# Performance work log

Measured on AMD Instinct MI355X. Metric: run time of the kernel, lower is better.

Reference implementation:

```python
import math
import jax, jax.numpy as jnp
import numpy as np

B, S, D = 4, 4096, 1024
H = 16
DH = D // H          # 64
INNER = H * DH       # 1024
EPS = 1e-6


def _layernorm(z, g, b):
    m = jnp.mean(z, axis=-1, keepdims=True)
    v = jnp.mean((z - m) ** 2, axis=-1, keepdims=True)
    return (z - m) * jax.lax.rsqrt(v + EPS) * g + b


def _pos_encoding(seq_len, d_model, dtype):
    pos = jnp.arange(seq_len, dtype=jnp.float32)[:, None]                    # [S,1]
    div = jnp.exp(jnp.arange(0, d_model, 2, dtype=jnp.float32)
                  * (-math.log(10000.0) / d_model))                          # [D/2]
    pe = jnp.zeros((seq_len, d_model), dtype=jnp.float32)
    pe = pe.at[:, 0::2].set(jnp.sin(pos * div))
    pe = pe.at[:, 1::2].set(jnp.cos(pos * div))
    return pe.astype(dtype)[None]                                            # [1,S,D]


def setup_inputs() -> dict:
    key = jax.random.key(0)
    ks = jax.random.split(key, 8)
    std = 0.02
    x = jax.random.normal(ks[0], (B, S, D), dtype=jnp.float32)
    inp = {
        "x": x,
        "ln1_g": jnp.ones((D,), jnp.float32),
        "ln1_b": jnp.zeros((D,), jnp.float32),
        "Wqkv": std * jax.random.normal(ks[1], (D, 3 * INNER), jnp.float32),
        "Wo": std * jax.random.normal(ks[2], (INNER, D), jnp.float32),
        "bo": jnp.zeros((D,), jnp.float32),
        "ln2_g": jnp.ones((D,), jnp.float32),
        "ln2_b": jnp.zeros((D,), jnp.float32),
        "W1": std * jax.random.normal(ks[3], (D, D), jnp.float32),
        "b1": jnp.zeros((D,), jnp.float32),
        "W2": std * jax.random.normal(ks[4], (D, D), jnp.float32),
        "b2": jnp.zeros((D,), jnp.float32),
    }
    return inp


def reference(x, ln1_g, ln1_b, Wqkv, Wo, bo, ln2_g, ln2_b, W1, b1, W2, b2):
    # --- ln_1 + positional encoding (dropout p=0) ---
    h = _layernorm(x, ln1_g, ln1_b)
    h = h + _pos_encoding(h.shape[1], h.shape[2], h.dtype)
    # --- linear self-attention (non-causal, efficient attention) ---
    qkv = h @ Wqkv                                                           # [B,S,3*INNER]
    q, k, v = jnp.split(qkv, 3, axis=-1)
    def heads(t):  # [B,S,INNER] -> [B,H,S,DH]
        return t.reshape(B, S, H, DH).transpose(0, 2, 1, 3)
    q, k, v = heads(q), heads(k), heads(v)
    q = jax.nn.softmax(q, axis=-1) * (DH ** -0.5)
    k = jax.nn.softmax(k, axis=-2)
    ctx = jnp.einsum("bhnd,bhne->bhde", k, v)                               # [B,H,DH,DH]
    attn_out = jnp.einsum("bhnd,bhde->bhne", q, ctx)                        # [B,H,S,DH]
    attn_out = attn_out.transpose(0, 2, 1, 3).reshape(B, S, INNER)
    attn_out = attn_out @ Wo + bo
    # --- residual, ln_2, MLP (Linear -> GELU -> Linear), residual ---
    x = x + attn_out
    y = _layernorm(x, ln2_g, ln2_b)
    y = jax.nn.gelu(y @ W1 + b1, approximate=False) @ W2 + b2
    return x + y
```

## Files before the change

### kernel.cpp

```cpp
#include <hip/hip_runtime.h>
#include <hip/hip_bf16.h>
#include <math.h>

#define B_   4
#define S_   4096
#define D_   1024
#define H_   16
#define DH_  64
#define BS_  (B_ * S_)
#define N3_  3072

using bf16 = __hip_bfloat16;
typedef __attribute__((ext_vector_type(8))) short bf16x8;
typedef __attribute__((ext_vector_type(4))) float f32x4;

#define GAS __attribute__((address_space(1)))
#define LAS __attribute__((address_space(3)))

__device__ __forceinline__ void gload_lds16(const bf16* g, bf16* l) {
  __builtin_amdgcn_global_load_lds((const GAS void*)g, (LAS void*)l, 16, 0, 0);
}

__device__ __forceinline__ float bf2f(short u) {
  unsigned int x = ((unsigned int)(unsigned short)u) << 16;
  return __builtin_bit_cast(float, x);
}
__device__ __forceinline__ unsigned short f2bfu(float f) {
  bf16 t = __float2bfloat16(f);
  return *(unsigned short*)&t;
}

__global__ __launch_bounds__(256)
void transpose_cast4(const float* __restrict__ Wqkv, const float* __restrict__ Wo,
                     const float* __restrict__ W1, const float* __restrict__ W2,
                     bf16* __restrict__ wqkvt, bf16* __restrict__ wot,
                     bf16* __restrict__ w1t, bf16* __restrict__ w2t)
{
  __shared__ float tile[32][33];
  int gx = blockIdx.x;
  const float* W; bf16* Wt; int N, xo;
  if (gx < 96)        { W = Wqkv; Wt = wqkvt; N = N3_; xo = gx; }
  else if (gx < 128)  { W = Wo;   Wt = wot;   N = D_;  xo = gx - 96; }
  else if (gx < 160)  { W = W1;   Wt = w1t;   N = D_;  xo = gx - 128; }
  else                { W = W2;   Wt = w2t;   N = D_;  xo = gx - 160; }
  int n0 = xo * 32, k0 = blockIdx.y * 32;
  int tx = threadIdx.x & 31, ty = threadIdx.x >> 5;
#pragma unroll
  for (int j = 0; j < 32; j += 8)
    tile[ty + j][tx] = W[(size_t)(k0 + ty + j) * N + n0 + tx];
  __syncthreads();
#pragma unroll
  for (int j = 0; j < 32; j += 8)
    Wt[(size_t)(n0 + ty + j) * 1024 + k0 + tx] = __float2bfloat16(tile[tx][ty + j]);
}

template<bool PE, bool INBF16>
__global__ __launch_bounds__(256)
void ln_kernel(const float* __restrict__ Xf, const bf16* __restrict__ Xb,
               const float* __restrict__ G, const float* __restrict__ Bv,
               bf16* __restrict__ out)
{
  int row = blockIdx.x;
  int t = threadIdx.x;
  float4 v;
  if (INBF16) {
    ushort4 u = ((const ushort4*)Xb)[(size_t)row * (D_ / 4) + t];
    v.x = bf2f(u.x); v.y = bf2f(u.y); v.z = bf2f(u.z); v.w = bf2f(u.w);
  } else {
    v = ((const float4*)(Xf + (size_t)row * D_))[t];
  }
  float s  = v.x + v.y + v.z + v.w;
  float ss = v.x * v.x + v.y * v.y + v.z * v.z + v.w * v.w;
#pragma unroll
  for (int o = 32; o > 0; o >>= 1) { s += __shfl_xor(s, o); ss += __shfl_xor(ss, o); }
  __shared__ float red[8];
  int wid = t >> 6, lane = t & 63;
  if (lane == 0) { red[wid] = s; red[4 + wid] = ss; }
  __syncthreads();
  s  = red[0] + red[1] + red[2] + red[3];
  ss = red[4] + red[5] + red[6] + red[7];
  float mean = s * (1.0f / D_);
  float var  = ss * (1.0f / D_) - mean * mean;
  float rs   = rsqrtf(var + 1e-6f);
  int d0 = t * 4;
  const float4 g4 = ((const float4*)G)[t];
  const float4 b4 = ((const float4*)Bv)[t];
  float o0 = (v.x - mean) * rs * g4.x + b4.x;
  float o1 = (v.y - mean) * rs * g4.y + b4.y;
  float o2 = (v.z - mean) * rs * g4.z + b4.z;
  float o3 = (v.w - mean) * rs * g4.w + b4.w;
  if (PE) {
    const float C = -0.0089944730194f;
    float p = (float)(row & (S_ - 1));
    float sn, cs;
    __sincosf(p * __expf((float)d0 * C), &sn, &cs);        o0 += sn; o1 += cs;
    __sincosf(p * __expf((float)(d0 + 2) * C), &sn, &cs);  o2 += sn; o3 += cs;
  }
  ushort4 pk;
  pk.x = f2bfu(o0); pk.y = f2bfu(o1); pk.z = f2bfu(o2); pk.w = f2bfu(o3);
  ((ushort4*)out)[(size_t)row * (D_ / 4) + t] = pk;
}

enum { EPI_QKV = 0, EPI_BIAS_RES_BF16 = 1, EPI_BIAS_GELU_BF16 = 2, EPI_BIAS_RESB_F32 = 3 };

#define MFMA_ __builtin_amdgcn_mfma_f32_16x16x32_bf16

template<int EPI, bool AHM>
__global__ __launch_bounds__(512)
void gemm256(const bf16* __restrict__ A, const bf16* __restrict__ Bt,
             float* __restrict__ Cf, bf16* __restrict__ Cb,
             const float* __restrict__ bias, const float* __restrict__ resf,
             const bf16* __restrict__ resb,
             bf16* __restrict__ Ck, bf16* __restrict__ Cv,
             int M, int N, int K)
{
  extern __shared__ __align__(16) char smem[];
  bf16* lds = (bf16*)smem;

  const int t = threadIdx.x;
  const int wid = t >> 6, lane = t & 63;
  const int wr = wid >> 2, wc = wid & 3;
  const int bid = blockIdx.x;
  const int c = bid & 7;
  const int w = bid >> 3;
  const int sst = w >> 4;
  const int ii = w & 15;
  const int txg = sst >> 1, tyg = sst & 1;
  const int iy = ii & 3, ix = ii >> 2;
  const int ty = c * 8 + tyg * 4 + iy;
  const int tx = txg * 4 + ix;
  const int m0 = ty << 8, n0 = tx << 8;

  const bf16* Ab = AHM
      ? A + (((size_t)(m0 >> 12) * 16) * 4096 + (m0 & 4095)) * 64
      : A + (size_t)m0 * K;
  const bf16* Bb = Bt + (size_t)n0 * K;

  const int srow = t >> 2;
  const int scol = (((t & 3) ^ ((t >> 3) & 3)) * 8);
  const int NT = K >> 6;
  const int fr = lane & 15;
  const int fksw = (((lane >> 4) ^ ((lane >> 1) & 3)) * 8);

  f32x4 acc[8][4] = {};

  #define LDSHALF(b, mat, kh) (lds + (((((b) << 1) + (mat)) << 1) + (kh)) * 8192)

  #define STAGE(kt, mat, kh) do {                                              \
    bf16* _dst = LDSHALF((kt) & 1, (mat), (kh)) + t * 8;                       \
    const int _ktk = (kt) & (NT - 1);                                          \
    if ((mat) == 0 && AHM) {                                                   \
      const bf16* _sb = Ab + (size_t)_ktk * 262144 + (size_t)srow * 64         \
                        + (kh) * 32 + scol;                                    \
      gload_lds16(_sb, _dst);                                                  \
      gload_lds16(_sb + 8192, _dst + 4096);                                    \
    } else {                                                                   \
      const bf16* _sb = ((mat) == 0 ? Ab : Bb) + (size_t)srow * K              \
                        + (_ktk << 6) + (kh) * 32 + scol;                      \
      gload_lds16(_sb, _dst);                                                  \
      gload_lds16(_sb + (size_t)128 * K, _dst + 4096);                         \
    }                                                                          \
  } while (0)

  STAGE(0, 0, 0); STAGE(0, 1, 0);
  STAGE(0, 0, 1); STAGE(0, 1, 1);
  asm volatile("s_waitcnt vmcnt(4)" ::: "memory");
  __builtin_amdgcn_s_barrier();

#pragma unroll 2
  for (int kt = 0; kt < NT; ++kt) {
    const int cur = kt & 1;
    const bf16* hA0 = LDSHALF(cur, 0, 0);
    const bf16* hB0 = LDSHALF(cur, 1, 0);
    const bf16* hA1 = LDSHALF(cur, 0, 1);
    const bf16* hB1 = LDSHALF(cur, 1, 1);
    bf16x8 a[8], b0, b1, b2, b3;

#pragma unroll
    for (int mi = 0; mi < 8; ++mi)
      a[mi] = *(const bf16x8*)&hA0[(wr * 128 + mi * 16 + fr) * 32 + fksw];
    b0 = *(const bf16x8*)&hB0[(wc * 64 +  0 + fr) * 32 + fksw];
    b1 = *(const bf16x8*)&hB0[(wc * 64 + 16 + fr) * 32 + fksw];
    STAGE(kt + 1, 0, 0);
    __builtin_amdgcn_s_barrier();
    __builtin_amdgcn_s_setprio(1);
#pragma unroll
    for (int mi = 0; mi < 8; ++mi) {
      acc[mi][0] = MFMA_(a[mi], b0, acc[mi][0], 0, 0, 0);
      acc[mi][1] = MFMA_(a[mi], b1, acc[mi][1], 0, 0, 0);
    }
    __builtin_amdgcn_s_setprio(0);
    __builtin_amdgcn_s_barrier();

    b2 = *(const bf16x8*)&hB0[(wc * 64 + 32 + fr) * 32 + fksw];
    b3 = *(const bf16x8*)&hB0[(wc * 64 + 48 + fr) * 32 + fksw];
    STAGE(kt + 1, 1, 0);
    __builtin_amdgcn_s_barrier();
    __builtin_amdgcn_s_setprio(1);
#pragma unroll
    for (int mi = 0; mi < 8; ++mi) {
      acc[mi][2] = MFMA_(a[mi], b2, acc[mi][2], 0, 0, 0);
      acc[mi][3] = MFMA_(a[mi], b3, acc[mi][3], 0, 0, 0);
    }
    __builtin_amdgcn_s_setprio(0);
    asm volatile("s_waitcnt vmcnt(4)" ::: "memory");
    __builtin_amdgcn_s_barrier();

#pragma unroll
    for (int mi = 0; mi < 8; ++mi)
      a[mi] = *(const bf16x8*)&hA1[(wr * 128 + mi * 16 + fr) * 32 + fksw];
    b0 = *(const bf16x8*)&hB1[(wc * 64 +  0 + fr) * 32 + fksw];
    b1 = *(const bf16x8*)&hB1[(wc * 64 + 16 + fr) * 32 + fksw];
    STAGE(kt + 1, 0, 1);
    __builtin_amdgcn_s_barrier();
    __builtin_amdgcn_s_setprio(1);
#pragma unroll
    for (int mi = 0; mi < 8; ++mi) {
      acc[mi][0] = MFMA_(a[mi], b0, acc[mi][0], 0, 0, 0);
      acc[mi][1] = MFMA_(a[mi], b1, acc[mi][1], 0, 0, 0);
    }
    __builtin_amdgcn_s_setprio(0);
    __builtin_amdgcn_s_barrier();

    b2 = *(const bf16x8*)&hB1[(wc * 64 + 32 + fr) * 32 + fksw];
    b3 = *(const bf16x8*)&hB1[(wc * 64 + 48 + fr) * 32 + fksw];
    STAGE(kt + 1, 1, 1);
    __builtin_amdgcn_s_barrier();
    __builtin_amdgcn_s_setprio(1);
#pragma unroll
    for (int mi = 0; mi < 8; ++mi) {
      acc[mi][2] = MFMA_(a[mi], b2, acc[mi][2], 0, 0, 0);
      acc[mi][3] = MFMA_(a[mi], b3, acc[mi][3], 0, 0, 0);
    }
    __builtin_amdgcn_s_setprio(0);
    asm volatile("s_waitcnt vmcnt(4)" ::: "memory");
    __builtin_amdgcn_s_barrier();
  }
  asm volatile("s_waitcnt vmcnt(0)" ::: "memory");

  const int brow = m0 >> 12;
  const int mrow = m0 & 4095;
#pragma unroll
  for (int mi = 0; mi < 8; ++mi) {
    int rowb = m0 + wr * 128 + mi * 16 + (lane >> 4) * 4;
#pragma unroll
    for (int ni = 0; ni < 4; ++ni) {
      int col = n0 + wc * 64 + ni * 16 + fr;
      if (EPI == EPI_QKV) {
        int qsel = col >> 10;
        int hh = (col >> 6) & 15;
        int dd = col & 63;
        int sloc = mrow + wr * 128 + mi * 16 + (lane >> 4) * 4;
        if (qsel == 0) {
          unsigned short* qp = (unsigned short*)Cb +
            (((size_t)(brow * 16 + hh) * 4096 + sloc) * 64 + dd);
#pragma unroll
          for (int j = 0; j < 4; ++j)
            qp[(size_t)j * 64] = f2bfu(acc[mi][ni][j]);
        } else {
          unsigned short* kp = (unsigned short*)(qsel == 1 ? Ck : Cv) +
            (((size_t)(brow * 16 + hh) * 64 + dd) * 4096 + sloc);
          ushort4 pk;
          pk.x = f2bfu(acc[mi][ni][0]); pk.y = f2bfu(acc[mi][ni][1]);
          pk.z = f2bfu(acc[mi][ni][2]); pk.w = f2bfu(acc[mi][ni][3]);
          *(ushort4*)kp = pk;
        }
      } else {
#pragma unroll
        for (int j = 0; j < 4; ++j) {
          int row = rowb + j;
          float v = acc[mi][ni][j];
          if (EPI == EPI_BIAS_RES_BF16) {
            Cb[(size_t)row * N + col] =
              __float2bfloat16(v + bias[col] + resf[(size_t)row * N + col]);
          } else if (EPI == EPI_BIAS_GELU_BF16) {
            float u = v + bias[col];
            u = 0.5f * u * (1.0f + erff(u * 0.70710678118654752f));
            Cb[(size_t)row * N + col] = __float2bfloat16(u);
          } else {
            Cf[(size_t)row * N + col] =
              v + bias[col] + bf2f(*(const short*)&resb[(size_t)row * N + col]);
          }
        }
      }
    }
  }
  #undef STAGE
  #undef LDSHALF
}

__global__ __launch_bounds__(256)
void ctx_partial(const bf16* __restrict__ kT, const bf16* __restrict__ vT,
                 float* __restrict__ pctx, float* __restrict__ pden)
{
  int blk = blockIdx.x;
  int kc = blk & 7, bh = blk >> 3;
  int t = threadIdx.x, lane = t & 63, wid = t >> 6;
  const int fr = lane & 15, g = lane >> 4;
  __shared__ float part[4][4096];
  __shared__ float dpart[4][64];

  f32x4 acc[4][4] = {};
  float dsum[4] = {0.f, 0.f, 0.f, 0.f};
  const unsigned short* kb = (const unsigned short*)kT + (size_t)bh * 64 * 4096;
  const unsigned short* vb = (const unsigned short*)vT + (size_t)bh * 64 * 4096;
  const int kbase = kc * 512 + wid * 128;
#pragma unroll
  for (int i = 0; i < 4; ++i) {
    int kofs = kbase + i * 32 + g * 8;
    bf16x8 av[4], bv[4];
#pragma unroll
    for (int mi = 0; mi < 4; ++mi) {
      bf16x8 kr = *(const bf16x8*)(kb + (size_t)(mi * 16 + fr) * 4096 + kofs);
      bf16x8 ae;
      float es = 0.f;
#pragma unroll
      for (int j = 0; j < 8; ++j) {
        float e = __expf(bf2f(kr[j]));
        es += e;
        ae[j] = (short)f2bfu(e);
      }
      dsum[mi] += es;
      av[mi] = ae;
      bv[mi] = *(const bf16x8*)(vb + (size_t)(mi * 16 + fr) * 4096 + kofs);
    }
#pragma unroll
    for (int mi = 0; mi < 4; ++mi)
#pragma unroll
      for (int ni = 0; ni < 4; ++ni)
        acc[mi][ni] = MFMA_(av[mi], bv[ni], acc[mi][ni], 0, 0, 0);
  }
#pragma unroll
  for (int mi = 0; mi < 4; ++mi) {
    dsum[mi] += __shfl_xor(dsum[mi], 16);
    dsum[mi] += __shfl_xor(dsum[mi], 32);
  }
#pragma unroll
  for (int mi = 0; mi < 4; ++mi)
#pragma unroll
    for (int ni = 0; ni < 4; ++ni)
      *(f32x4*)&part[wid][(mi * 4 + ni) * 256 + lane * 4] = acc[mi][ni];
  if (g == 0) {
#pragma unroll
    for (int mi = 0; mi < 4; ++mi) dpart[wid][mi * 16 + fr] = dsum[mi];
  }
  __syncthreads();
  int lane2 = t & 63, fg = t >> 6;
#pragma unroll
  for (int ff = 0; ff < 4; ++ff) {
    int f = fg * 4 + ff;
    f32x4 s = {};
#pragma unroll
    for (int ww = 0; ww < 4; ++ww)
      s += *(const f32x4*)&part[ww][f * 256 + lane2 * 4];
    *(f32x4*)&pctx[((size_t)blk * 16 + f) * 256 + lane2 * 4] = s;
  }
  if (t < 64)
    pden[blk * 64 + t] = dpart[0][t] + dpart[1][t] + dpart[2][t] + dpart[3][t];
}

__global__ __launch_bounds__(256)
void ctx_merge(const float* __restrict__ pctx, const float* __restrict__ pden,
               bf16* __restrict__ ctxT)
{
  int bh = blockIdx.x;
  int t = threadIdx.x, lane2 = t & 63, fg = t >> 6;
  __shared__ float rden[64];
  if (t < 64) {
    float s = 0.f;
    for (int kc = 0; kc < 8; ++kc) s += pden[(bh * 8 + kc) * 64 + t];
    rden[t] = 1.0f / s;
  }
  __syncthreads();
  int fr2 = lane2 & 15, g2 = lane2 >> 4;
#pragma unroll
  for (int ff = 0; ff < 4; ++ff) {
    int f = fg * 4 + ff;
    int mi = f >> 2, ni = f & 3;
    f32x4 s = {};
#pragma unroll
    for (int kc = 0; kc < 8; ++kc)
      s += *(const f32x4*)&pctx[(((size_t)(bh * 8 + kc)) * 16 + f) * 256 + lane2 * 4];
    int e = ni * 16 + fr2;
    int d0 = mi * 16 + g2 * 4;
    ushort4 pk;
    pk.x = f2bfu(s[0] * rden[d0 + 0]);
    pk.y = f2bfu(s[1] * rden[d0 + 1]);
    pk.z = f2bfu(s[2] * rden[d0 + 2]);
    pk.w = f2bfu(s[3] * rden[d0 + 3]);
    *(ushort4*)((unsigned short*)ctxT + ((size_t)bh * 64 + e) * 64 + d0) = pk;
  }
}

__global__ __launch_bounds__(256)
void attn_kernel(const bf16* __restrict__ qhm, const bf16* __restrict__ ctxT,
                 bf16* __restrict__ attn)
{
  int blk = blockIdx.x;
  int chunk = blk & 15, bh = blk >> 4;
  int t = threadIdx.x, lane = t & 63, wid = t >> 6;
  __shared__ bf16 P[256 * 64];
  __shared__ bf16 CT[64 * 64];

  {
    const unsigned short* cg = (const unsigned short*)ctxT + (size_t)bh * 4096;
#pragma unroll
    for (int r = 0; r < 2; ++r) {
      int idx = r * 256 + t;
      int e = idx >> 3, b = idx & 7;
      bf16x8 v = *(const bf16x8*)(cg + idx * 8);
      *(bf16x8*)&CT[e * 64 + ((b ^ (e & 7)) * 8)] = v;
    }
  }
  {
    int s = chunk * 256 + t;
    const unsigned short* qp = (const unsigned short*)qhm + ((size_t)bh * 4096 + s) * 64;
    float p[64];
#pragma unroll
    for (int j = 0; j < 8; ++j) {
      bf16x8 q8 = *(const bf16x8*)(qp + j * 8);
#pragma unroll
      for (int i = 0; i < 8; ++i) p[j * 8 + i] = bf2f(q8[i]);
    }
    float mx = p[0];
#pragma unroll
    for (int d = 1; d < 64; ++d) mx = fmaxf(mx, p[d]);
    float sum = 0.f;
#pragma unroll
    for (int d = 0; d < 64; ++d) { p[d] = __expf(p[d] - mx); sum += p[d]; }
    float f = 0.125f / sum;
    bf16* pb = &P[(t >> 6) * 4096 + (t & 63) * 64];
#pragma unroll
    for (int b = 0; b < 8; ++b) {
      bf16x8 pk;
#pragma unroll
      for (int i = 0; i < 8; ++i) pk[i] = (short)f2bfu(p[b * 8 + i] * f);
      *(bf16x8*)&pb[((b ^ (t & 7)) * 8)] = pk;
    }
  }
  __syncthreads();

  const int fr = lane & 15, g = lane >> 4;
  f32x4 acc[4][4] = {};
  const bf16* Pw = &P[wid * 4096];
#pragma unroll
  for (int ks = 0; ks < 2; ++ks) {
    bf16x8 av[4], bv[4];
#pragma unroll
    for (int mi = 0; mi < 4; ++mi) {
      int r = mi * 16 + fr;
      av[mi] = *(const bf16x8*)&Pw[r * 64 + (((ks * 4 + g) ^ (r & 7)) * 8)];
    }
#pragma unroll
    for (int ni = 0; ni < 4; ++ni) {
      int e = ni * 16 + fr;
      bv[ni] = *(const bf16x8*)&CT[e * 64 + (((ks * 4 + g) ^ (e & 7)) * 8)];
    }
#pragma unroll
    for (int mi = 0; mi < 4; ++mi)
#pragma unroll
      for (int ni = 0; ni < 4; ++ni)
        acc[mi][ni] = MFMA_(av[mi], bv[ni], acc[mi][ni], 0, 0, 0);
  }
  unsigned short* ob = (unsigned short*)attn +
      ((size_t)bh * 4096 + chunk * 256 + wid * 64) * 64;
#pragma unroll
  for (int mi = 0; mi < 4; ++mi)
#pragma unroll
    for (int ni = 0; ni < 4; ++ni) {
      int e = ni * 16 + fr;
#pragma unroll
      for (int j = 0; j < 4; ++j) {
        int r = mi * 16 + g * 4 + j;
        ob[(size_t)r * 64 + e] = f2bfu(acc[mi][ni][j]);
      }
    }
}

#define OFF_WQKVT  ((size_t)0)
#define OFF_WOT    ((size_t)6291456)
#define OFF_W1T    ((size_t)8388608)
#define OFF_W2T    ((size_t)10485760)
#define OFF_CTXT   ((size_t)12582912)
#define OFF_PCTX   ((size_t)13631488)
#define OFF_PDEN   ((size_t)22020096)
#define OFF_ATTN   ((size_t)33554432)
#define OFF_H      OFF_ATTN
#define OFF_QHM    ((size_t)67108864)
#define OFF_KT     ((size_t)100663296)
#define OFF_VT     ((size_t)134217728)
#define OFF_Z      OFF_QHM
#define OFF_X2B    OFF_KT
#define OFF_Y      OFF_VT

extern "C" void kernel_launch(void* const* d_in, const int* in_sizes, int n_in,
                              void* d_out, int out_size, void* d_ws, size_t ws_size,
                              hipStream_t stream)
{
  const float* x     = (const float*)d_in[0];
  const float* ln1_g = (const float*)d_in[1];
  const float* ln1_b = (const float*)d_in[2];
  const float* Wqkv  = (const float*)d_in[3];
  const float* Wo    = (const float*)d_in[4];
  const float* bo    = (const float*)d_in[5];
  const float* ln2_g = (const float*)d_in[6];
  const float* ln2_b = (const float*)d_in[7];
  const float* W1    = (const float*)d_in[8];
  const float* b1    = (const float*)d_in[9];
  const float* W2    = (const float*)d_in[10];
  const float* b2    = (const float*)d_in[11];
  float* out = (float*)d_out;
  char* ws = (char*)d_ws;

  bf16*  h     = (bf16*)(ws + OFF_H);
  bf16*  attn  = (bf16*)(ws + OFF_ATTN);
  bf16*  qhm   = (bf16*)(ws + OFF_QHM);
  bf16*  kT    = (bf16*)(ws + OFF_KT);
  bf16*  vT    = (bf16*)(ws + OFF_VT);
  bf16*  ctxT  = (bf16*)(ws + OFF_CTXT);
  float* pctx  = (float*)(ws + OFF_PCTX);
  float* pden  = (float*)(ws + OFF_PDEN);
  bf16*  x2b   = (bf16*)(ws + OFF_X2B);
  bf16*  y     = (bf16*)(ws + OFF_Y);
  bf16*  z     = (bf16*)(ws + OFF_Z);
  bf16*  wqkvt = (bf16*)(ws + OFF_WQKVT);
  bf16*  wot   = (bf16*)(ws + OFF_WOT);
  bf16*  w1t   = (bf16*)(ws + OFF_W1T);
  bf16*  w2t   = (bf16*)(ws + OFF_W2T);

  const size_t GEMM_LDS = 131072;

  transpose_cast4<<<dim3(192, 32), 256, 0, stream>>>(Wqkv, Wo, W1, W2,
                                                     wqkvt, wot, w1t, w2t);

  ln_kernel<true, false><<<BS_, 256, 0, stream>>>(x, nullptr, ln1_g, ln1_b, h);

  gemm256<EPI_QKV, false><<<(N3_ / 256) * (BS_ / 256), 512, GEMM_LDS, stream>>>(
      h, wqkvt, nullptr, qhm, nullptr, nullptr, nullptr, kT, vT, BS_, N3_, D_);

  ctx_partial<<<512, 256, 0, stream>>>(kT, vT, pctx, pden);
  ctx_merge<<<64, 256, 0, stream>>>(pctx, pden, ctxT);

  attn_kernel<<<1024, 256, 0, stream>>>(qhm, ctxT, attn);

  gemm256<EPI_BIAS_RES_BF16, true><<<(D_ / 256) * (BS_ / 256), 512, GEMM_LDS, stream>>>(
      attn, wot, nullptr, x2b, bo, x, nullptr, nullptr, nullptr, BS_, D_, D_);

  ln_kernel<false, true><<<BS_, 256, 0, stream>>>(nullptr, x2b, ln2_g, ln2_b, y);

  gemm256<EPI_BIAS_GELU_BF16, false><<<(D_ / 256) * (BS_ / 256), 512, GEMM_LDS, stream>>>(
      y, w1t, nullptr, z, b1, nullptr, nullptr, nullptr, nullptr, BS_, D_, D_);

  gemm256<EPI_BIAS_RESB_F32, false><<<(D_ / 256) * (BS_ / 256), 512, GEMM_LDS, stream>>>(
      z, w2t, out, nullptr, b2, nullptr, x2b, nullptr, nullptr, BS_, D_, D_);
}
```

Before: 353.6 us.

## Stage GEMM epilogues through LDS for vectorized stores; fuse LN1 with weight transpose

GEMM epilogues now write the bf16 accumulators into swizzled LDS, then read back rows of 8 elements so that bias, residual and GELU are applied and stored with 16-byte vector accesses instead of scalar strided writes. The Q part of the QKV GEMM uses the same path for head-major output. The first layernorm and the weight transpose-cast are merged into one launch. The prefetch index is clamped instead of wrapped. The trade-off is that intermediate results are rounded to bf16 before bias and residual are added, and the epilogue gains an extra LDS pass and a barrier.

```diff
diff --git a/kernel.cpp b/kernel.cpp
--- a/kernel.cpp
+++ b/kernel.cpp
@@ -31,44 +31,76 @@
 }
 
 __global__ __launch_bounds__(256)
-void transpose_cast4(const float* __restrict__ Wqkv, const float* __restrict__ Wo,
-                     const float* __restrict__ W1, const float* __restrict__ W2,
-                     bf16* __restrict__ wqkvt, bf16* __restrict__ wot,
-                     bf16* __restrict__ w1t, bf16* __restrict__ w2t)
+void prep_kernel(const float* __restrict__ x, const float* __restrict__ ln1_g,
+                 const float* __restrict__ ln1_b, bf16* __restrict__ h,
+                 const float* __restrict__ Wqkv, const float* __restrict__ Wo,
+                 const float* __restrict__ W1, const float* __restrict__ W2,
+                 bf16* __restrict__ wqkvt, bf16* __restrict__ wot,
+                 bf16* __restrict__ w1t, bf16* __restrict__ w2t)
 {
-  __shared__ float tile[32][33];
-  int gx = blockIdx.x;
-  const float* W; bf16* Wt; int N, xo;
-  if (gx < 96)        { W = Wqkv; Wt = wqkvt; N = N3_; xo = gx; }
-  else if (gx < 128)  { W = Wo;   Wt = wot;   N = D_;  xo = gx - 96; }
-  else if (gx < 160)  { W = W1;   Wt = w1t;   N = D_;  xo = gx - 128; }
-  else                { W = W2;   Wt = w2t;   N = D_;  xo = gx - 160; }
-  int n0 = xo * 32, k0 = blockIdx.y * 32;
-  int tx = threadIdx.x & 31, ty = threadIdx.x >> 5;
-#pragma unroll
-  for (int j = 0; j < 32; j += 8)
-    tile[ty + j][tx] = W[(size_t)(k0 + ty + j) * N + n0 + tx];
-  __syncthreads();
-#pragma unroll
-  for (int j = 0; j < 32; j += 8)
-    Wt[(size_t)(n0 + ty + j) * 1024 + k0 + tx] = __float2bfloat16(tile[tx][ty + j]);
-}
-
-template<bool PE, bool INBF16>
+  int bid = blockIdx.x;
+  int t = threadIdx.x;
+  if (bid < BS_) {
+    int row = bid;
+    float4 v = ((const float4*)(x + (size_t)row * D_))[t];
+    float s  = v.x + v.y + v.z + v.w;
+    float ss = v.x * v.x + v.y * v.y + v.z * v.z + v.w * v.w;
+#pragma unroll
+    for (int o = 32; o > 0; o >>= 1) { s += __shfl_xor(s, o); ss += __shfl_xor(ss, o); }
+    __shared__ float red[8];
+    int wid = t >> 6, lane = t & 63;
+    if (lane == 0) { red[wid] = s; red[4 + wid] = ss; }
+    __syncthreads();
+    s  = red[0] + red[1] + red[2] + red[3];
+    ss = red[4] + red[5] + red[6] + red[7];
+    float mean = s * (1.0f / D_);
+    float var  = ss * (1.0f / D_) - mean * mean;
+    float rs   = rsqrtf(var + 1e-6f);
+    int d0 = t * 4;
+    const float4 g4 = ((const float4*)ln1_g)[t];
+    const float4 b4 = ((const float4*)ln1_b)[t];
+    float o0 = (v.x - mean) * rs * g4.x + b4.x;
+    float o1 = (v.y - mean) * rs * g4.y + b4.y;
+    float o2 = (v.z - mean) * rs * g4.z + b4.z;
+    float o3 = (v.w - mean) * rs * g4.w + b4.w;
+    const float C = -0.0089944730194f;
+    float p = (float)(row & (S_ - 1));
+    float sn, cs;
+    __sincosf(p * __expf((float)d0 * C), &sn, &cs);        o0 += sn; o1 += cs;
+    __sincosf(p * __expf((float)(d0 + 2) * C), &sn, &cs);  o2 += sn; o3 += cs;
+    ushort4 pk;
+    pk.x = f2bfu(o0); pk.y = f2bfu(o1); pk.z = f2bfu(o2); pk.w = f2bfu(o3);
+    ((ushort4*)h)[(size_t)row * (D_ / 4) + t] = pk;
+  } else {
+    int e = bid - BS_;
+    int gx = e % 192, ky = e / 192;
+    __shared__ float tile[32][33];
+    const float* W; bf16* Wt; int N, xo;
+    if (gx < 96)        { W = Wqkv; Wt = wqkvt; N = N3_; xo = gx; }
+    else if (gx < 128)  { W = Wo;   Wt = wot;   N = D_;  xo = gx - 96; }
+    else if (gx < 160)  { W = W1;   Wt = w1t;   N = D_;  xo = gx - 128; }
+    else                { W = W2;   Wt = w2t;   N = D_;  xo = gx - 160; }
+    int n0 = xo * 32, k0 = ky * 32;
+    int tx = t & 31, ty = t >> 5;
+#pragma unroll
+    for (int j = 0; j < 32; j += 8)
+      tile[ty + j][tx] = W[(size_t)(k0 + ty + j) * N + n0 + tx];
+    __syncthreads();
+#pragma unroll
+    for (int j = 0; j < 32; j += 8)
+      Wt[(size_t)(n0 + ty + j) * 1024 + k0 + tx] = __float2bfloat16(tile[tx][ty + j]);
+  }
+}
+
 __global__ __launch_bounds__(256)
-void ln_kernel(const float* __restrict__ Xf, const bf16* __restrict__ Xb,
-               const float* __restrict__ G, const float* __restrict__ Bv,
-               bf16* __restrict__ out)
+void ln_kernel(const bf16* __restrict__ Xb, const float* __restrict__ G,
+               const float* __restrict__ Bv, bf16* __restrict__ out)
 {
   int row = blockIdx.x;
   int t = threadIdx.x;
+  ushort4 u = ((const ushort4*)Xb)[(size_t)row * (D_ / 4) + t];
   float4 v;
-  if (INBF16) {
-    ushort4 u = ((const ushort4*)Xb)[(size_t)row * (D_ / 4) + t];
-    v.x = bf2f(u.x); v.y = bf2f(u.y); v.z = bf2f(u.z); v.w = bf2f(u.w);
-  } else {
-    v = ((const float4*)(Xf + (size_t)row * D_))[t];
-  }
+  v.x = bf2f(u.x); v.y = bf2f(u.y); v.z = bf2f(u.z); v.w = bf2f(u.w);
   float s  = v.x + v.y + v.z + v.w;
   float ss = v.x * v.x + v.y * v.y + v.z * v.z + v.w * v.w;
 #pragma unroll
@@ -82,22 +114,13 @@
   float mean = s * (1.0f / D_);
   float var  = ss * (1.0f / D_) - mean * mean;
   float rs   = rsqrtf(var + 1e-6f);
-  int d0 = t * 4;
   const float4 g4 = ((const float4*)G)[t];
   const float4 b4 = ((const float4*)Bv)[t];
-  float o0 = (v.x - mean) * rs * g4.x + b4.x;
-  float o1 = (v.y - mean) * rs * g4.y + b4.y;
-  float o2 = (v.z - mean) * rs * g4.z + b4.z;
-  float o3 = (v.w - mean) * rs * g4.w + b4.w;
-  if (PE) {
-    const float C = -0.0089944730194f;
-    float p = (float)(row & (S_ - 1));
-    float sn, cs;
-    __sincosf(p * __expf((float)d0 * C), &sn, &cs);        o0 += sn; o1 += cs;
-    __sincosf(p * __expf((float)(d0 + 2) * C), &sn, &cs);  o2 += sn; o3 += cs;
-  }
   ushort4 pk;
-  pk.x = f2bfu(o0); pk.y = f2bfu(o1); pk.z = f2bfu(o2); pk.w = f2bfu(o3);
+  pk.x = f2bfu((v.x - mean) * rs * g4.x + b4.x);
+  pk.y = f2bfu((v.y - mean) * rs * g4.y + b4.y);
+  pk.z = f2bfu((v.z - mean) * rs * g4.z + b4.z);
+  pk.w = f2bfu((v.w - mean) * rs * g4.w + b4.w);
   ((ushort4*)out)[(size_t)row * (D_ / 4) + t] = pk;
 }
 
@@ -146,9 +169,9 @@
 
   #define LDSHALF(b, mat, kh) (lds + (((((b) << 1) + (mat)) << 1) + (kh)) * 8192)
 
-  #define STAGE(kt, mat, kh) do {                                              \
-    bf16* _dst = LDSHALF((kt) & 1, (mat), (kh)) + t * 8;                       \
-    const int _ktk = (kt) & (NT - 1);                                          \
+  #define STAGE(bkt, akt, mat, kh) do {                                        \
+    bf16* _dst = LDSHALF((bkt) & 1, (mat), (kh)) + t * 8;                      \
+    const int _ktk = (akt);                                                    \
     if ((mat) == 0 && AHM) {                                                   \
       const bf16* _sb = Ab + (size_t)_ktk * 262144 + (size_t)srow * 64         \
                         + (kh) * 32 + scol;                                    \
@@ -162,14 +185,15 @@
     }                                                                          \
   } while (0)
 
-  STAGE(0, 0, 0); STAGE(0, 1, 0);
-  STAGE(0, 0, 1); STAGE(0, 1, 1);
+  STAGE(0, 0, 0, 0); STAGE(0, 0, 1, 0);
+  STAGE(0, 0, 0, 1); STAGE(0, 0, 1, 1);
   asm volatile("s_waitcnt vmcnt(4)" ::: "memory");
   __builtin_amdgcn_s_barrier();
 
 #pragma unroll 2
   for (int kt = 0; kt < NT; ++kt) {
     const int cur = kt & 1;
+    const int nk = (kt + 1 < NT) ? (kt + 1) : (NT - 1);
     const bf16* hA0 = LDSHALF(cur, 0, 0);
     const bf16* hB0 = LDSHALF(cur, 1, 0);
     const bf16* hA1 = LDSHALF(cur, 0, 1);
@@ -181,7 +205,7 @@
       a[mi] = *(const bf16x8*)&hA0[(wr * 128 + mi * 16 + fr) * 32 + fksw];
     b0 = *(const bf16x8*)&hB0[(wc * 64 +  0 + fr) * 32 + fksw];
     b1 = *(const bf16x8*)&hB0[(wc * 64 + 16 + fr) * 32 + fksw];
-    STAGE(kt + 1, 0, 0);
+    STAGE(kt + 1, nk, 0, 0);
     __builtin_amdgcn_s_barrier();
     __builtin_amdgcn_s_setprio(1);
 #pragma unroll
@@ -194,7 +218,7 @@
 
     b2 = *(const bf16x8*)&hB0[(wc * 64 + 32 + fr) * 32 + fksw];
     b3 = *(const bf16x8*)&hB0[(wc * 64 + 48 + fr) * 32 + fksw];
-    STAGE(kt + 1, 1, 0);
+    STAGE(kt + 1, nk, 1, 0);
     __builtin_amdgcn_s_barrier();
     __builtin_amdgcn_s_setprio(1);
 #pragma unroll
@@ -211,7 +235,7 @@
       a[mi] = *(const bf16x8*)&hA1[(wr * 128 + mi * 16 + fr) * 32 + fksw];
     b0 = *(const bf16x8*)&hB1[(wc * 64 +  0 + fr) * 32 + fksw];
     b1 = *(const bf16x8*)&hB1[(wc * 64 + 16 + fr) * 32 + fksw];
-    STAGE(kt + 1, 0, 1);
+    STAGE(kt + 1, nk, 0, 1);
     __builtin_amdgcn_s_barrier();
     __builtin_amdgcn_s_setprio(1);
 #pragma unroll
@@ -224,7 +248,7 @@
 
     b2 = *(const bf16x8*)&hB1[(wc * 64 + 32 + fr) * 32 + fksw];
     b3 = *(const bf16x8*)&hB1[(wc * 64 + 48 + fr) * 32 + fksw];
-    STAGE(kt + 1, 1, 1);
+    STAGE(kt + 1, nk, 1, 1);
     __builtin_amdgcn_s_barrier();
     __builtin_amdgcn_s_setprio(1);
 #pragma unroll
@@ -238,26 +262,57 @@
   }
   asm volatile("s_waitcnt vmcnt(0)" ::: "memory");
 
-  const int brow = m0 >> 12;
-  const int mrow = m0 & 4095;
-#pragma unroll
-  for (int mi = 0; mi < 8; ++mi) {
-    int rowb = m0 + wr * 128 + mi * 16 + (lane >> 4) * 4;
-#pragma unroll
-    for (int ni = 0; ni < 4; ++ni) {
-      int col = n0 + wc * 64 + ni * 16 + fr;
-      if (EPI == EPI_QKV) {
-        int qsel = col >> 10;
-        int hh = (col >> 6) & 15;
-        int dd = col & 63;
+  unsigned short* ot = (unsigned short*)lds;
+
+  const bool q_repack = (EPI == EPI_QKV) && (n0 < 1024);
+  if (EPI != EPI_QKV || q_repack) {
+#pragma unroll
+    for (int mi = 0; mi < 8; ++mi) {
+#pragma unroll
+      for (int ni = 0; ni < 4; ++ni) {
+#pragma unroll
+        for (int j = 0; j < 4; ++j) {
+          int row = wr * 128 + mi * 16 + (lane >> 4) * 4 + j;
+          int col = wc * 64 + ni * 16 + fr;
+          int u = col >> 3;
+          int st = (u & ~7) | ((u ^ row) & 7);
+          ot[row * 256 + st * 8 + (col & 7)] = f2bfu(acc[mi][ni][j]);
+        }
+      }
+    }
+    __syncthreads();
+  }
+
+  if (EPI == EPI_QKV) {
+    const int brow = m0 >> 12;
+    const int mrow = m0 & 4095;
+    if (q_repack) {
+      int tq = t & 3, trow = t >> 2;
+#pragma unroll
+      for (int p = 0; p < 2; ++p) {
+        int row = p * 128 + trow;
+        int sglob = mrow + row;
+#pragma unroll
+        for (int i = 0; i < 8; ++i) {
+          int uu = i * 4 + tq;
+          int hl = uu >> 3, k = uu & 7;
+          int st = (uu & ~7) | ((uu ^ row) & 7);
+          bf16x8 v = *(const bf16x8*)&ot[row * 256 + st * 8];
+          unsigned short* dst = (unsigned short*)Cb +
+            (((size_t)(brow * 16 + (n0 >> 6) + hl) * 4096 + sglob) * 64 + k * 8);
+          *(bf16x8*)dst = v;
+        }
+      }
+    } else {
+      int qsel = n0 >> 10;
+#pragma unroll
+      for (int mi = 0; mi < 8; ++mi) {
         int sloc = mrow + wr * 128 + mi * 16 + (lane >> 4) * 4;
-        if (qsel == 0) {
-          unsigned short* qp = (unsigned short*)Cb +
-            (((size_t)(brow * 16 + hh) * 4096 + sloc) * 64 + dd);
-#pragma unroll
-          for (int j = 0; j < 4; ++j)
-            qp[(size_t)j * 64] = f2bfu(acc[mi][ni][j]);
-        } else {
+#pragma unroll
+        for (int ni = 0; ni < 4; ++ni) {
+          int col = n0 + wc * 64 + ni * 16 + fr;
+          int hh = (col >> 6) & 15;
+          int dd = col & 63;
           unsigned short* kp = (unsigned short*)(qsel == 1 ? Ck : Cv) +
             (((size_t)(brow * 16 + hh) * 64 + dd) * 4096 + sloc);
           ushort4 pk;
@@ -265,23 +320,52 @@
           pk.z = f2bfu(acc[mi][ni][2]); pk.w = f2bfu(acc[mi][ni][3]);
           *(ushort4*)kp = pk;
         }
+      }
+    }
+  } else {
+    int rlane = lane & 31;
+    int rrow0 = lane >> 5;
+    float bias8[8];
+    *(float4*)&bias8[0] = *(const float4*)&bias[n0 + rlane * 8];
+    *(float4*)&bias8[4] = *(const float4*)&bias[n0 + rlane * 8 + 4];
+#pragma unroll 4
+    for (int it = 0; it < 16; ++it) {
+      int row = wid * 32 + it * 2 + rrow0;
+      int st = (rlane & ~7) | ((rlane ^ row) & 7);
+      bf16x8 v8 = *(const bf16x8*)&ot[row * 256 + st * 8];
+      int grow = m0 + row;
+      float o[8];
+#pragma unroll
+      for (int q = 0; q < 8; ++q) o[q] = bf2f(v8[q]) + bias8[q];
+      if (EPI == EPI_BIAS_RES_BF16) {
+        const float* rp = resf + (size_t)grow * N + n0 + rlane * 8;
+        float4 r0 = *(const float4*)rp, r1 = *(const float4*)(rp + 4);
+        o[0] += r0.x; o[1] += r0.y; o[2] += r0.z; o[3] += r0.w;
+        o[4] += r1.x; o[5] += r1.y; o[6] += r1.z; o[7] += r1.w;
+        bf16x8 wv;
+#pragma unroll
+        for (int q = 0; q < 8; ++q) wv[q] = (short)f2bfu(o[q]);
+        *(bf16x8*)((unsigned short*)Cb + (size_t)grow * N + n0 + rlane * 8) = wv;
+      } else if (EPI == EPI_BIAS_GELU_BF16) {
+        bf16x8 wv;
+#pragma unroll
+        for (int q = 0; q < 8; ++q) {
+          float u = o[q];
+          u = 0.5f * u * (1.0f + erff(u * 0.70710678118654752f));
+          wv[q] = (short)f2bfu(u);
+        }
+        *(bf16x8*)((unsigned short*)Cb + (size_t)grow * N + n0 + rlane * 8) = wv;
       } else {
-#pragma unroll
-        for (int j = 0; j < 4; ++j) {
-          int row = rowb + j;
-          float v = acc[mi][ni][j];
-          if (EPI == EPI_BIAS_RES_BF16) {
-            Cb[(size_t)row * N + col] =
-              __float2bfloat16(v + bias[col] + resf[(size_t)row * N + col]);
-          } else if (EPI == EPI_BIAS_GELU_BF16) {
-            float u = v + bias[col];
-            u = 0.5f * u * (1.0f + erff(u * 0.70710678118654752f));
-            Cb[(size_t)row * N + col] = __float2bfloat16(u);
-          } else {
-            Cf[(size_t)row * N + col] =
-              v + bias[col] + bf2f(*(const short*)&resb[(size_t)row * N + col]);
-          }
-        }
+        const unsigned short* rp = (const unsigned short*)resb + (size_t)grow * N + n0 + rlane * 8;
+        bf16x8 r8 = *(const bf16x8*)rp;
+#pragma unroll
+        for (int q = 0; q < 8; ++q) o[q] += bf2f(r8[q]);
+        float4 s0, s1;
+        s0.x = o[0]; s0.y = o[1]; s0.z = o[2]; s0.w = o[3];
+        s1.x = o[4]; s1.y = o[5]; s1.z = o[6]; s1.w = o[7];
+        float* op = Cf + (size_t)grow * N + n0 + rlane * 8;
+        *(float4*)op = s0;
+        *(float4*)(op + 4) = s1;
       }
     }
   }
@@ -530,10 +614,8 @@
 
   const size_t GEMM_LDS = 131072;
 
-  transpose_cast4<<<dim3(192, 32), 256, 0, stream>>>(Wqkv, Wo, W1, W2,
-                                                     wqkvt, wot, w1t, w2t);
-
-  ln_kernel<true, false><<<BS_, 256, 0, stream>>>(x, nullptr, ln1_g, ln1_b, h);
+  prep_kernel<<<BS_ + 192 * 32, 256, 0, stream>>>(
+      x, ln1_g, ln1_b, h, Wqkv, Wo, W1, W2, wqkvt, wot, w1t, w2t);
 
   gemm256<EPI_QKV, false><<<(N3_ / 256) * (BS_ / 256), 512, GEMM_LDS, stream>>>(
       h, wqkvt, nullptr, qhm, nullptr, nullptr, nullptr, kT, vT, BS_, N3_, D_);
@@ -546,7 +628,7 @@
   gemm256<EPI_BIAS_RES_BF16, true><<<(D_ / 256) * (BS_ / 256), 512, GEMM_LDS, stream>>>(
       attn, wot, nullptr, x2b, bo, x, nullptr, nullptr, nullptr, BS_, D_, D_);
 
-  ln_kernel<false, true><<<BS_, 256, 0, stream>>>(nullptr, x2b, ln2_g, ln2_b, y);
+  ln_kernel<<<BS_, 256, 0, stream>>>(x2b, ln2_g, ln2_b, y);
 
   gemm256<EPI_BIAS_GELU_BF16, false><<<(D_ / 256) * (BS_ / 256), 512, GEMM_LDS, stream>>>(
       y, w1t, nullptr, z, b1, nullptr, nullptr, nullptr, nullptr, BS_, D_, D_);
```

Result: no change. 350.7 us (-0.8%).
